# Performance work log

Measured on AMD Instinct MI355X. Metric: run time of the kernel, lower is better.

## Reference

```python
import jax, jax.numpy as jnp
import numpy as np

MARGIN = 0.075
CONF_THRESHOLD = 0.2


def setup_inputs() -> dict:
    key = jax.random.key(0)
    k1, k2, k3 = jax.random.split(key, 3)
    N, D = 32768, 256
    embeddings = jax.random.normal(k1, (N, D), dtype=jnp.float32)
    tags = jax.random.randint(k2, (N,), 0, 500, dtype=jnp.int64)
    confidences = jax.random.uniform(k3, (N,), dtype=jnp.float32)
    return {"embeddings": embeddings, "tags": tags, "confidences": confidences}


def _safe_sqrt(sq):
    # gradient-safe sqrt: zero at sq<=0 (matches d(0)=0, avoids NaN in vjp)
    pos = sq > 0
    return jnp.where(pos, jnp.sqrt(jnp.where(pos, sq, 1.0)), 0.0)


def _triplet_hard_mining(emb, labels):
    n = emb.shape[0]
    # pairwise euclidean distances (cdist p=2)
    sq_norm = jnp.sum(emb * emb, axis=1)  # [n]
    sq = sq_norm[:, None] + sq_norm[None, :] - 2.0 * (emb @ emb.T)
    dist = _safe_sqrt(jnp.maximum(sq, 0.0))  # [n, n]

    same = labels[:, None] == labels[None, :]
    eye = jnp.eye(n, dtype=bool)
    pos_mask = same & ~eye
    neg_mask = ~same

    inf = jnp.float32(jnp.inf)
    hard_pos = jnp.max(jnp.where(pos_mask, dist, -inf), axis=1)  # [n]
    neg_min = jnp.min(jnp.where(neg_mask, dist, inf), axis=1)    # [n]
    # semi-hard negatives: neg dists strictly greater than hardest positive
    shn_mask = neg_mask & (dist > hard_pos[:, None])
    shn_min = jnp.min(jnp.where(shn_mask, dist, inf), axis=1)
    hard_neg = jnp.where(jnp.isfinite(shn_min), shn_min, neg_min)

    valid = jnp.any(pos_mask, axis=1) & jnp.any(neg_mask, axis=1)
    per_anchor = jax.nn.relu(hard_pos - hard_neg + MARGIN)
    per_anchor = jnp.where(valid, per_anchor, 0.0)
    cnt = jnp.sum(valid.astype(jnp.float32))
    # if no valid anchors (also covers <2 unique labels), loss is 0
    return jnp.where(cnt > 0, jnp.sum(per_anchor) / jnp.maximum(cnt, 1.0), 0.0)


def reference(embeddings, tags, confidences):
    n = embeddings.shape[0]
    top_k = int(CONF_THRESHOLD * n)
    _, idx = jax.lax.top_k(confidences, top_k)
    emb = embeddings[idx]
    labels = tags[idx]
    return _triplet_hard_mining(emb, labels)
```

## Files before the change

kernel.cpp:

```cpp
#include <hip/hip_runtime.h>
#include <math.h>

#define D 256
#define MARGIN 0.075f
#define MAXM 96

typedef __bf16 bf8_t __attribute__((ext_vector_type(8)));
typedef float f4_t __attribute__((ext_vector_type(4)));
typedef int i4_t __attribute__((ext_vector_type(4)));
typedef unsigned long long ull;

#define AS1 __attribute__((address_space(1)))
#define AS3 __attribute__((address_space(3)))
static __device__ __forceinline__ void gload_lds16(const void* g, void* s) {
    __builtin_amdgcn_global_load_lds((const AS1 unsigned int*)g, (AS3 unsigned int*)s, 16, 0, 0);
}

static __device__ __forceinline__ unsigned short f2bf(float x) {
    unsigned u = __float_as_uint(x);
    unsigned r = (u + 0x7fffu + ((u >> 16) & 1u)) >> 16;
    return (unsigned short)r;
}

static __device__ __forceinline__ float dec_min(unsigned cm) {
    return (cm == 0u) ? __builtin_inff() : __uint_as_float(~cm);
}

static __device__ __forceinline__ float rmin16(float v) {
    int s;
    s = __builtin_amdgcn_update_dpp(__float_as_int(v), __float_as_int(v), 0x101, 0xF, 0xF, false);
    v = fminf(v, __int_as_float(s));
    s = __builtin_amdgcn_update_dpp(__float_as_int(v), __float_as_int(v), 0x102, 0xF, 0xF, false);
    v = fminf(v, __int_as_float(s));
    s = __builtin_amdgcn_update_dpp(__float_as_int(v), __float_as_int(v), 0x104, 0xF, 0xF, false);
    v = fminf(v, __int_as_float(s));
    s = __builtin_amdgcn_update_dpp(__float_as_int(v), __float_as_int(v), 0x108, 0xF, 0xF, false);
    v = fminf(v, __int_as_float(s));
    return v;
}

__global__ __launch_bounds__(256) void k_histscan(const float* __restrict__ conf,
                                                  int n, int ksel,
                                                  unsigned* __restrict__ h1,
                                                  unsigned* __restrict__ ctrl) {
    int t = threadIdx.x;
    int i = blockIdx.x * 256 + t;
    if (i < n) atomicAdd(&h1[__float_as_uint(conf[i]) >> 16], 1u);
    __threadfence();
    __syncthreads();
    __shared__ unsigned sdone;
    if (t == 0) sdone = atomicAdd(&ctrl[8], 1u);
    __syncthreads();
    if (sdone != gridDim.x - 1) return;
    __threadfence();
    __shared__ unsigned part[256], sfx[256];
    __shared__ int schunk;
    unsigned k = (unsigned)ksel;
    unsigned s = 0;
    const uint4* h4 = (const uint4*)(h1 + t * 256);
    #pragma unroll
    for (int b = 0; b < 64; b++) { uint4 v = h4[b]; s += v.x + v.y + v.z + v.w; }
    part[t] = s;
    __syncthreads();
    for (int off = 1; off < 256; off <<= 1) {
        unsigned v = (t + off < 256) ? part[t + off] : 0u;
        __syncthreads();
        part[t] += v;
        __syncthreads();
    }
    if (part[t] >= k && (t == 255 || part[t + 1] < k)) schunk = t;
    __syncthreads();
    int c = schunk;
    unsigned above = (c == 255) ? 0u : part[c + 1];
    sfx[t] = h1[c * 256 + t];
    __syncthreads();
    for (int off = 1; off < 256; off <<= 1) {
        unsigned v = (t + off < 256) ? sfx[t + off] : 0u;
        __syncthreads();
        sfx[t] += v;
        __syncthreads();
    }
    if (above + sfx[t] >= k && (t == 255 || above + sfx[t + 1] < k)) {
        unsigned gt = above + ((t == 255) ? 0u : sfx[t + 1]);
        ctrl[3] = (unsigned)(c * 256 + t);
        ctrl[1] = gt;
        ctrl[2] = k - gt;
    }
}

__global__ __launch_bounds__(256) void k_selrank(const float* __restrict__ conf, int n,
                                                 unsigned* __restrict__ ctrl,
                                                 int* __restrict__ idx_sel,
                                                 ull* __restrict__ cand) {
    int t = threadIdx.x;
    int i = blockIdx.x * 256 + t;
    unsigned b16 = ctrl[3];
    if (i < n) {
        unsigned u = __float_as_uint(conf[i]);
        unsigned t16 = u >> 16;
        if (t16 > b16) {
            unsigned pos = atomicAdd(&ctrl[5], 1u);
            idx_sel[pos] = i;
        } else if (t16 == b16) {
            unsigned pos = atomicAdd(&ctrl[6], 1u);
            __hip_atomic_store(&cand[pos], ((ull)u << 32) | (unsigned)i,
                               __ATOMIC_RELAXED, __HIP_MEMORY_SCOPE_AGENT);
        }
    }
    __threadfence();
    __syncthreads();
    __shared__ unsigned sdone;
    if (t == 0) sdone = atomicAdd(&ctrl[9], 1u);
    __syncthreads();
    if (sdone != gridDim.x - 1) return;
    __threadfence();

    __shared__ ull scand[1024];
    int M = (int)__hip_atomic_load(&ctrl[6], __ATOMIC_RELAXED, __HIP_MEMORY_SCOPE_AGENT);
    unsigned need = ctrl[2], cgt = ctrl[1];
    bool useLds = (M <= 1024);
    if (useLds) {
        for (int m = t; m < M; m += 256)
            scand[m] = __hip_atomic_load(&cand[m], __ATOMIC_RELAXED, __HIP_MEMORY_SCOPE_AGENT);
        __syncthreads();
    }
    for (int j = t; j < M; j += 256) {
        ull cj = useLds ? scand[j]
                        : __hip_atomic_load(&cand[j], __ATOMIC_RELAXED, __HIP_MEMORY_SCOPE_AGENT);
        unsigned uj = (unsigned)(cj >> 32);
        unsigned rank = 0;
        for (int m = 0; m < M; m++) {
            ull cm = useLds ? scand[m]
                            : __hip_atomic_load(&cand[m], __ATOMIC_RELAXED, __HIP_MEMORY_SCOPE_AGENT);
            unsigned um = (unsigned)(cm >> 32);
            if (um > uj || (um == uj && cm < cj)) rank++;
        }
        if (rank < need) idx_sel[cgt + rank] = (int)(unsigned)(cj & 0xFFFFFFFFu);
    }
}

__global__ void k_gather(const float* __restrict__ emb, const int* __restrict__ tags,
                         const int* __restrict__ idx_sel, int ksel, int np,
                         unsigned short* __restrict__ ebf, float* __restrict__ sqn,
                         int* __restrict__ lsel, unsigned* __restrict__ labhist,
                         int* __restrict__ members) {
    int j = blockIdx.x;
    int t = threadIdx.x;
    if (j < ksel) {
        int src = idx_sel[j];
        float4 v = *(const float4*)&emb[(size_t)src * D + t * 4];
        ushort4 o;
        o.x = f2bf(v.x); o.y = f2bf(v.y); o.z = f2bf(v.z); o.w = f2bf(v.w);
        *(ushort4*)&ebf[(size_t)j * D + t * 4] = o;
        float s = v.x * v.x + v.y * v.y + v.z * v.z + v.w * v.w;
        for (int off = 32; off > 0; off >>= 1) s += __shfl_down(s, off);
        if (t == 0) {
            int lab = tags[src];
            sqn[j] = s; lsel[j] = lab;
            unsigned slot = atomicAdd(&labhist[lab], 1u);
            if (slot < MAXM) members[lab * MAXM + slot] = j;
        }
    } else {
        ushort4 z = {0, 0, 0, 0};
        *(ushort4*)&ebf[(size_t)j * D + t * 4] = z;
        if (t == 0) { sqn[j] = __builtin_inff(); lsel[j] = -1; }
    }
}

__global__ __launch_bounds__(256) void k_hardpos(const unsigned short* __restrict__ ebf,
                                                 const float* __restrict__ sqn,
                                                 const int* __restrict__ members,
                                                 const unsigned* __restrict__ labhist,
                                                 unsigned* __restrict__ hp_g) {
    int L = blockIdx.x;
    int t = threadIdx.x;
    int m = (int)labhist[L];
    if (m > MAXM) m = MAXM;
    if (m < 2) return;

    __shared__ unsigned short rows[MAXM * 256];
    __shared__ float lsqn[MAXM];
    __shared__ unsigned hpl[MAXM];
    __shared__ int ridx[MAXM];

    for (int a = t; a < m; a += 256) {
        int r = members[L * MAXM + a];
        ridx[a] = r; lsqn[a] = sqn[r]; hpl[a] = 0u;
    }
    __syncthreads();
    for (int e = t * 8; e < m * 256; e += 256 * 8) {
        int a = e >> 8, c = e & 255;
        *(uint4*)&rows[a * 256 + c] = *(const uint4*)&ebf[(size_t)ridx[a] * D + c];
    }
    __syncthreads();

    int npair = m * (m - 1) / 2;
    for (int pidx = t; pidx < npair; pidx += 256) {
        int a = 0, rem = pidx;
        while (rem >= m - 1 - a) { rem -= m - 1 - a; a++; }
        int b = a + 1 + rem;
        const unsigned* ra = (const unsigned*)&rows[a * 256];
        const unsigned* rb = (const unsigned*)&rows[b * 256];
        float dot = 0.f;
        #pragma unroll 8
        for (int c = 0; c < 128; c++) {
            unsigned ua = ra[c], ub = rb[c];
            float a0 = __uint_as_float(ua << 16);
            float a1 = __uint_as_float(ua & 0xFFFF0000u);
            float b0 = __uint_as_float(ub << 16);
            float b1 = __uint_as_float(ub & 0xFFFF0000u);
            dot = fmaf(a0, b0, dot);
            dot = fmaf(a1, b1, dot);
        }
        float dsq = fmaxf(lsqn[a] + lsqn[b] - 2.f * dot, 0.f);
        unsigned bits = __float_as_uint(dsq);
        atomicMax(&hpl[a], bits);
        atomicMax(&hpl[b], bits);
    }
    __syncthreads();
    for (int a = t; a < m; a += 256) hp_g[ridx[a]] = hpl[a];
}

__global__ __launch_bounds__(256, 3) void k_fused(const unsigned short* __restrict__ Ebf,
                                                  const float* __restrict__ sqn,
                                                  const int* __restrict__ lsel,
                                                  const unsigned* __restrict__ hp_g,
                                                  unsigned* __restrict__ nm_g,
                                                  unsigned* __restrict__ shn_g,
                                                  int np, int nb, int ksel) {
    int rem = blockIdx.x, bi = 0;
    while (rem >= nb - bi) { rem -= nb - bi; bi++; }
    int bj = bi + rem;
    int i0 = bi * 128, j0 = bj * 128;
    bool diag = (bi == bj);

    __shared__ __align__(16) char smem[32768];
    char* ldsA = smem;
    char* ldsB = smem + 16384;

    int t = threadIdx.x;
    int w = t >> 6, l = t & 63;
    int wm = w & 1, wn = w >> 1;
    int lr = l & 15, lq = l >> 4;
    int r7 = lr & 7, rh = lr >> 3;

    int dr = l >> 3;
    int sg = (l & 7) ^ dr;
    const unsigned short* gA = Ebf + (size_t)(i0 + dr) * D + sg * 8;
    const unsigned short* gB = Ebf + (size_t)(j0 + dr) * D + sg * 8;

    f4_t zero = {0.f, 0.f, 0.f, 0.f};
    f4_t acc[4][4];
    #pragma unroll
    for (int p = 0; p < 4; p++)
        #pragma unroll
        for (int q = 0; q < 4; q++) acc[p][q] = zero;

    for (int k0 = 0; k0 < D; k0 += 64) {
        #pragma unroll
        for (int c = 0; c < 4; c++) {
            int R0 = w * 32 + c * 8;
            gload_lds16(gA + (size_t)R0 * D + k0, ldsA + R0 * 128);
            gload_lds16(gB + (size_t)R0 * D + k0, ldsB + R0 * 128);
        }
        __syncthreads();
        #pragma unroll
        for (int ks8 = 0; ks8 < 8; ks8 += 4) {
            bf8_t a[4], b[4];
            #pragma unroll
            for (int p = 0; p < 4; p++) {
                int off = ((wm * 8 + p * 2 + rh) << 10) + ((r7 * 8 + ((ks8 + lq) ^ r7)) << 4);
                a[p] = *(const bf8_t*)(ldsA + off);
            }
            #pragma unroll
            for (int q = 0; q < 4; q++) {
                int off = ((wn * 8 + q * 2 + rh) << 10) + ((r7 * 8 + ((ks8 + lq) ^ r7)) << 4);
                b[q] = *(const bf8_t*)(ldsB + off);
            }
            #pragma unroll
            for (int p = 0; p < 4; p++)
                #pragma unroll
                for (int q = 0; q < 4; q++)
                    acc[p][q] = __builtin_amdgcn_mfma_f32_16x16x32_bf16(a[p], b[q], acc[p][q], 0, 0, 0);
        }
        __syncthreads();
    }

    float* sqnA = (float*)smem;
    float* sqnB = sqnA + 128;
    int* labA = (int*)(sqnB + 128);
    int* labB = labA + 128;
    float* thrA = (float*)(labB + 128);
    float* thrB = thrA + 128;
    if (t < 128) {
        float s = sqn[i0 + t];
        sqnA[t] = s; labA[t] = lsel[i0 + t];
        thrA[t] = __uint_as_float(hp_g[i0 + t]) - s;
    } else {
        int u = t - 128;
        float s = sqn[j0 + u];
        sqnB[u] = s; labB[u] = lsel[j0 + u];
        thrB[u] = __uint_as_float(hp_g[j0 + u]) - s;
    }
    __syncthreads();

    const float INF = __builtin_inff();
    int colL[4], ljv[4];
    float sBq[4], thrBq[4];
    #pragma unroll
    for (int q = 0; q < 4; q++) {
        colL[q] = wn * 64 + q * 16 + lr;
        ljv[q] = labB[colL[q]];
        sBq[q] = sqnB[colL[q]];
        thrBq[q] = thrB[colL[q]];
    }
    f4_t sqA4[4], thrA4[4];
    i4_t labA4[4];
    #pragma unroll
    for (int p = 0; p < 4; p++) {
        int rb = wm * 64 + p * 16 + lq * 4;
        sqA4[p] = *(const f4_t*)&sqnA[rb];
        thrA4[p] = *(const f4_t*)&thrA[rb];
        labA4[p] = *(const i4_t*)&labA[rb];
    }

    #pragma unroll
    for (int p = 0; p < 4; p++) {
        #pragma unroll
        for (int r = 0; r < 4; r++) {
            int li = labA4[p][r];
            float thr = thrA4[p][r];
            float nmv = INF, smv = INF;
            #pragma unroll
            for (int q = 0; q < 4; q++) {
                float v = fmaf(-2.f, acc[p][q][r], sBq[q]);
                v = (ljv[q] == li) ? INF : v;
                nmv = fminf(nmv, v);
                smv = fminf(smv, (v > thr) ? v : INF);
            }
            nmv = rmin16(nmv);
            smv = rmin16(smv);
            if (lr == 0) {
                int gm = i0 + wm * 64 + p * 16 + lq * 4 + r;
                float sqi = sqA4[p][r];
                if (nmv < INF)
                    atomicMax(&nm_g[gm], ~__float_as_uint(fmaxf(sqi + nmv, 0.f)));
                if (smv < INF)
                    atomicMax(&shn_g[gm], ~__float_as_uint(fmaxf(sqi + smv, 0.f)));
            }
        }
    }

    if (!diag) {
        #pragma unroll
        for (int q = 0; q < 4; q++) {
            int lj = ljv[q];
            float thrc = thrBq[q];
            float nmv = INF, smv = INF;
            #pragma unroll
            for (int p = 0; p < 4; p++)
                #pragma unroll
                for (int r = 0; r < 4; r++) {
                    float w2 = fmaf(-2.f, acc[p][q][r], sqA4[p][r]);
                    w2 = (labA4[p][r] == lj) ? INF : w2;
                    nmv = fminf(nmv, w2);
                    smv = fminf(smv, (w2 > thrc) ? w2 : INF);
                }
            nmv = fminf(nmv, __shfl_xor(nmv, 16));
            nmv = fminf(nmv, __shfl_xor(nmv, 32));
            smv = fminf(smv, __shfl_xor(smv, 16));
            smv = fminf(smv, __shfl_xor(smv, 32));
            if (lq == 0) {
                int gn = j0 + colL[q];
                if (nmv < INF)
                    atomicMax(&nm_g[gn], ~__float_as_uint(fmaxf(sBq[q] + nmv, 0.f)));
                if (smv < INF)
                    atomicMax(&shn_g[gn], ~__float_as_uint(fmaxf(sBq[q] + smv, 0.f)));
            }
        }
    }
}

__global__ __launch_bounds__(256) void k_loss(const unsigned* __restrict__ hp,
                                              const unsigned* __restrict__ nm,
                                              const unsigned* __restrict__ shn,
                                              const int* __restrict__ lsel,
                                              const unsigned* __restrict__ labhist,
                                              int ksel, float* __restrict__ fsums,
                                              unsigned* __restrict__ ctrl,
                                              float* __restrict__ out) {
    __shared__ float ssum[256], scnt[256];
    int t = threadIdx.x;
    int i = blockIdx.x * 256 + t;
    float sum = 0.f, cnt = 0.f;
    if (i < ksel) {
        int li = lsel[i];
        unsigned h = labhist[li];
        bool valid = (h >= 2u) && ((unsigned)ksel > h);
        float hp2 = __uint_as_float(hp[i]);
        float nm2 = dec_min(nm[i]);
        float sh2 = dec_min(shn[i]);
        float hn2 = isinf(sh2) ? nm2 : sh2;
        float lv = valid ? fmaxf(sqrtf(hp2) - sqrtf(hn2) + MARGIN, 0.f) : 0.f;
        sum = lv;
        cnt = valid ? 1.f : 0.f;
    }
    ssum[t] = sum; scnt[t] = cnt;
    __syncthreads();
    for (int off = 128; off > 0; off >>= 1) {
        if (t < off) { ssum[t] += ssum[t + off]; scnt[t] += scnt[t + off]; }
        __syncthreads();
    }
    if (t == 0) {
        atomicAdd(&fsums[0], ssum[0]);
        atomicAdd(&fsums[1], scnt[0]);
        __threadfence();
        unsigned done = atomicAdd(&ctrl[7], 1u);
        if (done == gridDim.x - 1) {
            float s = atomicAdd(&fsums[0], 0.f);
            float c = atomicAdd(&fsums[1], 0.f);
            out[0] = (c > 0.f) ? (s / fmaxf(c, 1.f)) : 0.f;
        }
    }
}

__global__ void k_wsfail(float* out, float code) { out[0] = code; }

static inline size_t align_up(size_t x, size_t a) { return (x + a - 1) & ~(a - 1); }

extern "C" void kernel_launch(void* const* d_in, const int* in_sizes, int n_in,
                              void* d_out, int out_size, void* d_ws, size_t ws_size,
                              hipStream_t stream) {
    const float* emb  = (const float*)d_in[0];
    const int*   tags = (const int*)d_in[1];
    const float* conf = (const float*)d_in[2];
    float* out = (float*)d_out;

    int n = in_sizes[2];
    int ksel = (int)(0.2 * (double)n);
    int np = ((ksel + 127) / 128) * 128;
    int nb = np / 128;
    int nlab = 512;

    size_t off = 0;
    size_t o_ctrl = off; off = align_up(off + 32 * sizeof(unsigned), 256);
    size_t o_fs   = off; off = align_up(off + 8 * sizeof(float), 256);
    size_t o_lh   = off; off = align_up(off + (size_t)nlab * 4, 256);
    size_t o_hp   = off; off = align_up(off + (size_t)np * 4, 256);
    size_t o_nm   = off; off = align_up(off + (size_t)np * 4, 256);
    size_t o_shn  = off; off = align_up(off + (size_t)np * 4, 256);
    size_t o_h1   = off; off = align_up(off + 65536 * 4, 256);
    size_t zero_bytes = off;
    size_t o_idx  = off; off = align_up(off + (size_t)ksel * 4, 256);
    size_t o_cand = off; off = align_up(off + (size_t)n * 8, 256);
    size_t o_mem  = off; off = align_up(off + (size_t)nlab * MAXM * 4, 256);
    size_t o_lab  = off; off = align_up(off + (size_t)np * 4, 256);
    size_t o_sqn  = off; off = align_up(off + (size_t)np * 4, 256);
    size_t o_ebf  = off; off = align_up(off + (size_t)np * D * 2, 256);

    if (ws_size < off) {
        k_wsfail<<<1, 1, 0, stream>>>(out, -(float)(ws_size >> 20));
        return;
    }

    char* ws = (char*)d_ws;
    unsigned*       ctrl    = (unsigned*)(ws + o_ctrl);
    float*          fsums   = (float*)(ws + o_fs);
    unsigned*       labhist = (unsigned*)(ws + o_lh);
    unsigned*       hp_g    = (unsigned*)(ws + o_hp);
    unsigned*       nm_g    = (unsigned*)(ws + o_nm);
    unsigned*       shn_g   = (unsigned*)(ws + o_shn);
    unsigned*       h1      = (unsigned*)(ws + o_h1);
    int*            idx_sel = (int*)(ws + o_idx);
    ull*            cand    = (ull*)(ws + o_cand);
    int*            members = (int*)(ws + o_mem);
    int*            lsel    = (int*)(ws + o_lab);
    float*          sqn     = (float*)(ws + o_sqn);
    unsigned short* ebf     = (unsigned short*)(ws + o_ebf);

    hipMemsetAsync(d_ws, 0, zero_bytes, stream);
    int selgrid = (n + 255) / 256;
    k_histscan<<<selgrid, 256, 0, stream>>>(conf, n, ksel, h1, ctrl);
    k_selrank<<<selgrid, 256, 0, stream>>>(conf, n, ctrl, idx_sel, cand);
    k_gather<<<np, 64, 0, stream>>>(emb, tags, idx_sel, ksel, np, ebf, sqn, lsel,
                                    labhist, members);
    k_hardpos<<<512, 256, 0, stream>>>(ebf, sqn, members, labhist, hp_g);
    int ntri = nb * (nb + 1) / 2;
    k_fused<<<ntri, 256, 0, stream>>>(ebf, sqn, lsel, hp_g, nm_g, shn_g, np, nb, ksel);
    k_loss<<<(ksel + 255) / 256, 256, 0, stream>>>(hp_g, nm_g, shn_g, lsel, labhist,
                                                   ksel, fsums, ctrl, out);
}
```

Baseline: 194.4 us.

## Fuse loss into tile kernel, aggregate mins in LDS, widen selection blocks

Several changes land together. The final loss reduction now runs in the last block of the fused distance kernel via a completion counter, which removes one kernel launch and the float atomics. Per-tile row and column minima are first combined in shared memory with ordered-uint atomics, then written once per row or column to global memory, cutting global atomic traffic. The histogram and select kernels move to 1024-thread blocks and the second-level scan becomes a serial 64-bin walk, and the gather kernel packs four rows per block. The costs are extra shared memory per tile and a serialized final reduction in a single block.

After: 238.0 us. 22.4% more time.

```diff
diff --git a/kernel.cpp b/kernel.cpp
--- a/kernel.cpp
+++ b/kernel.cpp
@@ -24,6 +24,15 @@
 
 static __device__ __forceinline__ float dec_min(unsigned cm) {
     return (cm == 0u) ? __builtin_inff() : __uint_as_float(~cm);
+}
+
+static __device__ __forceinline__ unsigned f2ord(float x) {
+    unsigned u = __float_as_uint(x);
+    return (u >> 31) ? ~u : (u ^ 0x80000000u);
+}
+static __device__ __forceinline__ float ord2f(unsigned o) {
+    unsigned u = (o & 0x80000000u) ? (o ^ 0x80000000u) : ~o;
+    return __uint_as_float(u);
 }
 
 static __device__ __forceinline__ float rmin16(float v) {
@@ -39,12 +48,12 @@
     return v;
 }
 
-__global__ __launch_bounds__(256) void k_histscan(const float* __restrict__ conf,
-                                                  int n, int ksel,
-                                                  unsigned* __restrict__ h1,
-                                                  unsigned* __restrict__ ctrl) {
+__global__ __launch_bounds__(1024) void k_histscan(const float* __restrict__ conf,
+                                                   int n, int ksel,
+                                                   unsigned* __restrict__ h1,
+                                                   unsigned* __restrict__ ctrl) {
     int t = threadIdx.x;
-    int i = blockIdx.x * 256 + t;
+    int i = blockIdx.x * 1024 + t;
     if (i < n) atomicAdd(&h1[__float_as_uint(conf[i]) >> 16], 1u);
     __threadfence();
     __syncthreads();
@@ -53,47 +62,44 @@
     __syncthreads();
     if (sdone != gridDim.x - 1) return;
     __threadfence();
-    __shared__ unsigned part[256], sfx[256];
+    __shared__ unsigned part[1024];
     __shared__ int schunk;
     unsigned k = (unsigned)ksel;
     unsigned s = 0;
-    const uint4* h4 = (const uint4*)(h1 + t * 256);
+    const uint4* h4 = (const uint4*)(h1 + t * 64);
     #pragma unroll
-    for (int b = 0; b < 64; b++) { uint4 v = h4[b]; s += v.x + v.y + v.z + v.w; }
+    for (int b = 0; b < 16; b++) { uint4 v = h4[b]; s += v.x + v.y + v.z + v.w; }
     part[t] = s;
     __syncthreads();
-    for (int off = 1; off < 256; off <<= 1) {
-        unsigned v = (t + off < 256) ? part[t + off] : 0u;
+    for (int off = 1; off < 1024; off <<= 1) {
+        unsigned v = (t + off < 1024) ? part[t + off] : 0u;
         __syncthreads();
         part[t] += v;
         __syncthreads();
     }
-    if (part[t] >= k && (t == 255 || part[t + 1] < k)) schunk = t;
-    __syncthreads();
-    int c = schunk;
-    unsigned above = (c == 255) ? 0u : part[c + 1];
-    sfx[t] = h1[c * 256 + t];
-    __syncthreads();
-    for (int off = 1; off < 256; off <<= 1) {
-        unsigned v = (t + off < 256) ? sfx[t + off] : 0u;
-        __syncthreads();
-        sfx[t] += v;
-        __syncthreads();
-    }
-    if (above + sfx[t] >= k && (t == 255 || above + sfx[t + 1] < k)) {
-        unsigned gt = above + ((t == 255) ? 0u : sfx[t + 1]);
-        ctrl[3] = (unsigned)(c * 256 + t);
-        ctrl[1] = gt;
-        ctrl[2] = k - gt;
-    }
-}
-
-__global__ __launch_bounds__(256) void k_selrank(const float* __restrict__ conf, int n,
-                                                 unsigned* __restrict__ ctrl,
-                                                 int* __restrict__ idx_sel,
-                                                 ull* __restrict__ cand) {
+    if (part[t] >= k && (t == 1023 || part[t + 1] < k)) schunk = t;
+    __syncthreads();
+    if (t == 0) {
+        int c = schunk;
+        unsigned cum = (c == 1023) ? 0u : part[c + 1];
+        int bin = 0; unsigned rem = 1;
+        for (int b = 63; b >= 0; b--) {
+            unsigned h = h1[c * 64 + b];
+            if (cum + h >= k) { bin = c * 64 + b; rem = k - cum; break; }
+            cum += h;
+        }
+        ctrl[3] = (unsigned)bin;
+        ctrl[1] = k - rem;
+        ctrl[2] = rem;
+    }
+}
+
+__global__ __launch_bounds__(1024) void k_selrank(const float* __restrict__ conf, int n,
+                                                  unsigned* __restrict__ ctrl,
+                                                  int* __restrict__ idx_sel,
+                                                  ull* __restrict__ cand) {
     int t = threadIdx.x;
-    int i = blockIdx.x * 256 + t;
+    int i = blockIdx.x * 1024 + t;
     unsigned b16 = ctrl[3];
     if (i < n) {
         unsigned u = __float_as_uint(conf[i]);
@@ -120,11 +126,11 @@
     unsigned need = ctrl[2], cgt = ctrl[1];
     bool useLds = (M <= 1024);
     if (useLds) {
-        for (int m = t; m < M; m += 256)
+        for (int m = t; m < M; m += 1024)
             scand[m] = __hip_atomic_load(&cand[m], __ATOMIC_RELAXED, __HIP_MEMORY_SCOPE_AGENT);
         __syncthreads();
     }
-    for (int j = t; j < M; j += 256) {
+    for (int j = t; j < M; j += 1024) {
         ull cj = useLds ? scand[j]
                         : __hip_atomic_load(&cand[j], __ATOMIC_RELAXED, __HIP_MEMORY_SCOPE_AGENT);
         unsigned uj = (unsigned)(cj >> 32);
@@ -139,31 +145,36 @@
     }
 }
 
-__global__ void k_gather(const float* __restrict__ emb, const int* __restrict__ tags,
-                         const int* __restrict__ idx_sel, int ksel, int np,
-                         unsigned short* __restrict__ ebf, float* __restrict__ sqn,
-                         int* __restrict__ lsel, unsigned* __restrict__ labhist,
-                         int* __restrict__ members) {
-    int j = blockIdx.x;
+__global__ __launch_bounds__(256) void k_gather(const float* __restrict__ emb,
+                                                const int* __restrict__ tags,
+                                                const int* __restrict__ idx_sel,
+                                                int ksel, int np,
+                                                unsigned short* __restrict__ ebf,
+                                                float* __restrict__ sqn,
+                                                int* __restrict__ lsel,
+                                                unsigned* __restrict__ labhist,
+                                                int* __restrict__ members) {
     int t = threadIdx.x;
+    int j = blockIdx.x * 4 + (t >> 6);
+    int lane = t & 63;
     if (j < ksel) {
         int src = idx_sel[j];
-        float4 v = *(const float4*)&emb[(size_t)src * D + t * 4];
+        float4 v = *(const float4*)&emb[(size_t)src * D + lane * 4];
         ushort4 o;
         o.x = f2bf(v.x); o.y = f2bf(v.y); o.z = f2bf(v.z); o.w = f2bf(v.w);
-        *(ushort4*)&ebf[(size_t)j * D + t * 4] = o;
+        *(ushort4*)&ebf[(size_t)j * D + lane * 4] = o;
         float s = v.x * v.x + v.y * v.y + v.z * v.z + v.w * v.w;
         for (int off = 32; off > 0; off >>= 1) s += __shfl_down(s, off);
-        if (t == 0) {
+        if (lane == 0) {
             int lab = tags[src];
             sqn[j] = s; lsel[j] = lab;
             unsigned slot = atomicAdd(&labhist[lab], 1u);
             if (slot < MAXM) members[lab * MAXM + slot] = j;
         }
-    } else {
+    } else if (j < np) {
         ushort4 z = {0, 0, 0, 0};
-        *(ushort4*)&ebf[(size_t)j * D + t * 4] = z;
-        if (t == 0) { sqn[j] = __builtin_inff(); lsel[j] = -1; }
+        *(ushort4*)&ebf[(size_t)j * D + lane * 4] = z;
+        if (lane == 0) { sqn[j] = __builtin_inff(); lsel[j] = -1; }
     }
 }
 
@@ -227,7 +238,10 @@
                                                   const unsigned* __restrict__ hp_g,
                                                   unsigned* __restrict__ nm_g,
                                                   unsigned* __restrict__ shn_g,
-                                                  int np, int nb, int ksel) {
+                                                  int np, int nb, int ksel,
+                                                  const unsigned* __restrict__ labhist,
+                                                  unsigned* __restrict__ ctrl,
+                                                  float* __restrict__ out) {
     int rem = blockIdx.x, bi = 0;
     while (rem >= nb - bi) { rem -= nb - bi; bi++; }
     int bj = bi + rem;
@@ -292,6 +306,10 @@
     int* labB = labA + 128;
     float* thrA = (float*)(labB + 128);
     float* thrB = thrA + 128;
+    unsigned* rowNm = (unsigned*)(thrB + 128);
+    unsigned* rowSh = rowNm + 128;
+    unsigned* colNm = rowSh + 128;
+    unsigned* colSh = colNm + 128;
     if (t < 128) {
         float s = sqn[i0 + t];
         sqnA[t] = s; labA[t] = lsel[i0 + t];
@@ -302,24 +320,29 @@
         sqnB[u] = s; labB[u] = lsel[j0 + u];
         thrB[u] = __uint_as_float(hp_g[j0 + u]) - s;
     }
+    rowNm[t & 127] = 0xFFFFFFFFu;
+    rowSh[t & 127] = 0xFFFFFFFFu;
+    colNm[t & 127] = 0xFFFFFFFFu;
+    colSh[t & 127] = 0xFFFFFFFFu;
     __syncthreads();
 
     const float INF = __builtin_inff();
     int colL[4], ljv[4];
-    float sBq[4], thrBq[4];
+    float thrBq[4];
     #pragma unroll
     for (int q = 0; q < 4; q++) {
         colL[q] = wn * 64 + q * 16 + lr;
         ljv[q] = labB[colL[q]];
-        sBq[q] = sqnB[colL[q]];
         thrBq[q] = thrB[colL[q]];
     }
-    f4_t sqA4[4], thrA4[4];
+    float sBq[4];
+    #pragma unroll
+    for (int q = 0; q < 4; q++) sBq[q] = sqnB[colL[q]];
+    f4_t thrA4[4];
     i4_t labA4[4];
     #pragma unroll
     for (int p = 0; p < 4; p++) {
         int rb = wm * 64 + p * 16 + lq * 4;
-        sqA4[p] = *(const f4_t*)&sqnA[rb];
         thrA4[p] = *(const f4_t*)&thrA[rb];
         labA4[p] = *(const i4_t*)&labA[rb];
     }
@@ -341,12 +364,9 @@
             nmv = rmin16(nmv);
             smv = rmin16(smv);
             if (lr == 0) {
-                int gm = i0 + wm * 64 + p * 16 + lq * 4 + r;
-                float sqi = sqA4[p][r];
-                if (nmv < INF)
-                    atomicMax(&nm_g[gm], ~__float_as_uint(fmaxf(sqi + nmv, 0.f)));
-                if (smv < INF)
-                    atomicMax(&shn_g[gm], ~__float_as_uint(fmaxf(sqi + smv, 0.f)));
+                int rowL = wm * 64 + p * 16 + lq * 4 + r;
+                if (nmv < INF) atomicMin(&rowNm[rowL], f2ord(nmv));
+                if (smv < INF) atomicMin(&rowSh[rowL], f2ord(smv));
             }
         }
     }
@@ -361,66 +381,66 @@
             for (int p = 0; p < 4; p++)
                 #pragma unroll
                 for (int r = 0; r < 4; r++) {
-                    float w2 = fmaf(-2.f, acc[p][q][r], sqA4[p][r]);
+                    float w2 = fmaf(-2.f, acc[p][q][r], sqnA[wm * 64 + p * 16 + lq * 4 + r]);
                     w2 = (labA4[p][r] == lj) ? INF : w2;
                     nmv = fminf(nmv, w2);
                     smv = fminf(smv, (w2 > thrc) ? w2 : INF);
                 }
-            nmv = fminf(nmv, __shfl_xor(nmv, 16));
-            nmv = fminf(nmv, __shfl_xor(nmv, 32));
-            smv = fminf(smv, __shfl_xor(smv, 16));
-            smv = fminf(smv, __shfl_xor(smv, 32));
-            if (lq == 0) {
-                int gn = j0 + colL[q];
-                if (nmv < INF)
-                    atomicMax(&nm_g[gn], ~__float_as_uint(fmaxf(sBq[q] + nmv, 0.f)));
-                if (smv < INF)
-                    atomicMax(&shn_g[gn], ~__float_as_uint(fmaxf(sBq[q] + smv, 0.f)));
-            }
-        }
-    }
-}
-
-__global__ __launch_bounds__(256) void k_loss(const unsigned* __restrict__ hp,
-                                              const unsigned* __restrict__ nm,
-                                              const unsigned* __restrict__ shn,
-                                              const int* __restrict__ lsel,
-                                              const unsigned* __restrict__ labhist,
-                                              int ksel, float* __restrict__ fsums,
-                                              unsigned* __restrict__ ctrl,
-                                              float* __restrict__ out) {
-    __shared__ float ssum[256], scnt[256];
-    int t = threadIdx.x;
-    int i = blockIdx.x * 256 + t;
-    float sum = 0.f, cnt = 0.f;
-    if (i < ksel) {
-        int li = lsel[i];
-        unsigned h = labhist[li];
-        bool valid = (h >= 2u) && ((unsigned)ksel > h);
-        float hp2 = __uint_as_float(hp[i]);
-        float nm2 = dec_min(nm[i]);
-        float sh2 = dec_min(shn[i]);
-        float hn2 = isinf(sh2) ? nm2 : sh2;
-        float lv = valid ? fmaxf(sqrtf(hp2) - sqrtf(hn2) + MARGIN, 0.f) : 0.f;
-        sum = lv;
-        cnt = valid ? 1.f : 0.f;
-    }
-    ssum[t] = sum; scnt[t] = cnt;
-    __syncthreads();
-    for (int off = 128; off > 0; off >>= 1) {
-        if (t < off) { ssum[t] += ssum[t + off]; scnt[t] += scnt[t + off]; }
+            if (nmv < INF) atomicMin(&colNm[colL[q]], f2ord(nmv));
+            if (smv < INF) atomicMin(&colSh[colL[q]], f2ord(smv));
+        }
+    }
+    __syncthreads();
+
+    if (t < 128) {
+        float sqi = sqnA[t];
+        float v = ord2f(rowNm[t]);
+        if (isfinite(v)) atomicMax(&nm_g[i0 + t], ~__float_as_uint(fmaxf(sqi + v, 0.f)));
+        float v2 = ord2f(rowSh[t]);
+        if (isfinite(v2)) atomicMax(&shn_g[i0 + t], ~__float_as_uint(fmaxf(sqi + v2, 0.f)));
+    } else if (!diag) {
+        int u = t - 128;
+        float sqj = sqnB[u];
+        float v = ord2f(colNm[u]);
+        if (isfinite(v)) atomicMax(&nm_g[j0 + u], ~__float_as_uint(fmaxf(sqj + v, 0.f)));
+        float v2 = ord2f(colSh[u]);
+        if (isfinite(v2)) atomicMax(&shn_g[j0 + u], ~__float_as_uint(fmaxf(sqj + v2, 0.f)));
+    }
+
+    __shared__ unsigned sflag;
+    __syncthreads();
+    if (t == 0) {
+        __threadfence();
+        unsigned d = __hip_atomic_fetch_add(&ctrl[7], 1u, __ATOMIC_ACQ_REL,
+                                            __HIP_MEMORY_SCOPE_AGENT);
+        sflag = (d == (unsigned)(gridDim.x - 1)) ? 1u : 0u;
+    }
+    __syncthreads();
+    if (sflag) {
+        float* ssum = (float*)smem;
+        float* scnt = ssum + 256;
+        float sum = 0.f, cnt = 0.f;
+        for (int i = t; i < ksel; i += 256) {
+            int li = lsel[i];
+            unsigned h = labhist[li];
+            bool valid = (h >= 2u) && ((unsigned)ksel > h);
+            float hp2 = __uint_as_float(hp_g[i]);
+            float nm2 = dec_min(__hip_atomic_load(&nm_g[i], __ATOMIC_RELAXED,
+                                                  __HIP_MEMORY_SCOPE_AGENT));
+            float sh2 = dec_min(__hip_atomic_load(&shn_g[i], __ATOMIC_RELAXED,
+                                                  __HIP_MEMORY_SCOPE_AGENT));
+            float hn2 = isinf(sh2) ? nm2 : sh2;
+            float lv = valid ? fmaxf(sqrtf(hp2) - sqrtf(hn2) + MARGIN, 0.f) : 0.f;
+            sum += lv;
+            cnt += valid ? 1.f : 0.f;
+        }
+        ssum[t] = sum; scnt[t] = cnt;
         __syncthreads();
-    }
-    if (t == 0) {
-        atomicAdd(&fsums[0], ssum[0]);
-        atomicAdd(&fsums[1], scnt[0]);
-        __threadfence();
-        unsigned done = atomicAdd(&ctrl[7], 1u);
-        if (done == gridDim.x - 1) {
-            float s = atomicAdd(&fsums[0], 0.f);
-            float c = atomicAdd(&fsums[1], 0.f);
-            out[0] = (c > 0.f) ? (s / fmaxf(c, 1.f)) : 0.f;
-        }
+        for (int off = 128; off > 0; off >>= 1) {
+            if (t < off) { ssum[t] += ssum[t + off]; scnt[t] += scnt[t + off]; }
+            __syncthreads();
+        }
+        if (t == 0) out[0] = (scnt[0] > 0.f) ? (ssum[0] / fmaxf(scnt[0], 1.f)) : 0.f;
     }
 }
 
@@ -444,7 +464,6 @@
 
     size_t off = 0;
     size_t o_ctrl = off; off = align_up(off + 32 * sizeof(unsigned), 256);
-    size_t o_fs   = off; off = align_up(off + 8 * sizeof(float), 256);
     size_t o_lh   = off; off = align_up(off + (size_t)nlab * 4, 256);
     size_t o_hp   = off; off = align_up(off + (size_t)np * 4, 256);
     size_t o_nm   = off; off = align_up(off + (size_t)np * 4, 256);
@@ -465,7 +484,6 @@
 
     char* ws = (char*)d_ws;
     unsigned*       ctrl    = (unsigned*)(ws + o_ctrl);
-    float*          fsums   = (float*)(ws + o_fs);
     unsigned*       labhist = (unsigned*)(ws + o_lh);
     unsigned*       hp_g    = (unsigned*)(ws + o_hp);
     unsigned*       nm_g    = (unsigned*)(ws + o_nm);
@@ -479,14 +497,13 @@
     unsigned short* ebf     = (unsigned short*)(ws + o_ebf);
 
     hipMemsetAsync(d_ws, 0, zero_bytes, stream);
-    int selgrid = (n + 255) / 256;
-    k_histscan<<<selgrid, 256, 0, stream>>>(conf, n, ksel, h1, ctrl);
-    k_selrank<<<selgrid, 256, 0, stream>>>(conf, n, ctrl, idx_sel, cand);
-    k_gather<<<np, 64, 0, stream>>>(emb, tags, idx_sel, ksel, np, ebf, sqn, lsel,
-                                    labhist, members);
+    int selgrid = (n + 1023) / 1024;
+    k_histscan<<<selgrid, 1024, 0, stream>>>(conf, n, ksel, h1, ctrl);
+    k_selrank<<<selgrid, 1024, 0, stream>>>(conf, n, ctrl, idx_sel, cand);
+    k_gather<<<np / 4, 256, 0, stream>>>(emb, tags, idx_sel, ksel, np, ebf, sqn, lsel,
+                                         labhist, members);
     k_hardpos<<<512, 256, 0, stream>>>(ebf, sqn, members, labhist, hp_g);
     int ntri = nb * (nb + 1) / 2;
-    k_fused<<<ntri, 256, 0, stream>>>(ebf, sqn, lsel, hp_g, nm_g, shn_g, np, nb, ksel);
-    k_loss<<<(ksel + 255) / 256, 256, 0, stream>>>(hp_g, nm_g, shn_g, lsel, labhist,
-                                                   ksel, fsums, ctrl, out);
-}
+    k_fused<<<ntri, 256, 0, stream>>>(ebf, sqn, lsel, hp_g, nm_g, shn_g, np, nb, ksel,
+                                      labhist, ctrl, out);
+}
```
